# Kernel optimization log

Hardware: AMD Instinct MI355X
Metric: run time of the kernel (lower is better)

The kernel has to match this reference:

```python
import jax, jax.numpy as jnp
import numpy as np

DIM = 256
HEADS = 4
DIM_HEADS = 32
HIDDEN = HEADS * DIM_HEADS


def setup_inputs() -> dict:
    key = jax.random.key(0)
    k0, k1, k2, k3, k4, k5, k6 = jax.random.split(key, 7)
    b, c, h, w = 16, DIM, 64, 64
    s = 1.0 / np.sqrt(DIM)
    return {
        "x": jax.random.normal(k0, (b, c, h, w), dtype=jnp.float32),
        "Wq": jax.random.normal(k1, (HIDDEN, DIM), dtype=jnp.float32) * s,
        "Wk": jax.random.normal(k2, (HIDDEN, DIM), dtype=jnp.float32) * s,
        "Wv": jax.random.normal(k3, (HIDDEN, DIM), dtype=jnp.float32) * s,
        "Wo": jax.random.normal(k4, (DIM, HIDDEN), dtype=jnp.float32) / np.sqrt(HIDDEN),
        "bo": jax.random.normal(k5, (DIM,), dtype=jnp.float32) * 0.01,
        "g": jnp.ones((DIM,), dtype=jnp.float32),
    }


def reference(x, Wq, Wk, Wv, Wo, bo, g):
    b, c, h, w = x.shape
    n = h * w
    scale = DIM_HEADS ** (-0.5)
    xf = x.reshape(b, c, n)  # [b,c,n]
    # 1x1 convs == channel matmuls
    q = jnp.einsum('dc,bcn->bdn', Wq, xf).reshape(b, HEADS, DIM_HEADS, n)
    k = jnp.einsum('dc,bcn->bdn', Wk, xf).reshape(b, HEADS, DIM_HEADS, n)
    v = jnp.einsum('dc,bcn->bdn', Wv, xf).reshape(b, HEADS, DIM_HEADS, n)
    q = jax.nn.softmax(q, axis=-2) * scale  # softmax over head-dim
    k = jax.nn.softmax(k, axis=-1)          # softmax over tokens
    v = v / n
    context = jnp.einsum('bhdn,bhen->bhde', k, v)  # [b,h,dh,dh]
    out = jnp.einsum('bhde,bhdn->bhen', context, q)  # [b,h,dh,n]
    out = out.reshape(b, HIDDEN, n)
    out = jnp.einsum('cd,bdn->bcn', Wo, out) + bo[None, :, None]
    # LayerNorm over channel dim (biased var, eps=1e-5 for fp32)
    eps = 1e-5
    mean = jnp.mean(out, axis=1, keepdims=True)
    var = jnp.var(out, axis=1, keepdims=True)
    out = (out - mean) * jax.lax.rsqrt(var + eps) * g[None, :, None]
    return out.reshape(b, c, h, w)
```

## Files before the change

kernel.cpp:

```cpp
#include <hip/hip_runtime.h>
#include <hip/hip_bf16.h>

typedef float f32x4 __attribute__((ext_vector_type(4)));
typedef short bf16x8 __attribute__((ext_vector_type(8)));
typedef unsigned short us4 __attribute__((ext_vector_type(4)));

#define NB 16
#define NC 256
#define NTOK 4096
#define NHID 128

__device__ __forceinline__ unsigned pk2(float lo, float hi) {
  float2 f; f.x = lo; f.y = hi;
  __hip_bfloat162 h = __float22bfloat162_rn(f);
  unsigned u; __builtin_memcpy(&u, &h, 4); return u;
}
__device__ __forceinline__ uint2 pk4(f32x4 v) {
  uint2 r; r.x = pk2(v[0], v[1]); r.y = pk2(v[2], v[3]); return r;
}
__device__ __forceinline__ float bf2f(unsigned short h) {
  union { unsigned u; float f; } v; v.u = ((unsigned)h) << 16;
  return v.f;
}

__global__ __launch_bounds__(512) void k0_w(
    const float* __restrict__ Wq, const float* __restrict__ Wk,
    const float* __restrict__ Wv, unsigned short* __restrict__ Wswz)
{
  const int mt = blockIdx.x;
  const int t = threadIdx.x;
  const int ks = t >> 6, l = t & 63;
  const int m = mt * 16 + (l & 15);
  const int col = ks * 32 + (l >> 4) * 8;
  const float* src = (m < 128) ? (Wq + (size_t)m * NC)
                   : (m < 256) ? (Wk + (size_t)(m - 128) * NC)
                               : (Wv + (size_t)(m - 256) * NC);
  const float4 w0 = *(const float4*)(src + col);
  const float4 w1 = *(const float4*)(src + col + 4);
  uint4 p;
  p.x = pk2(w0.x, w0.y); p.y = pk2(w0.z, w0.w);
  p.z = pk2(w1.x, w1.y); p.w = pk2(w1.z, w1.w);
  *(uint4*)&Wswz[((size_t)(mt * 8 + ks)) * 512 + l * 8] = p;
}

__global__ __launch_bounds__(512, 6) void k1_qkv(
    const float* __restrict__ x, const unsigned short* __restrict__ Wswz,
    unsigned short* __restrict__ qg, unsigned short* __restrict__ Pp,
    float* __restrict__ Sp)
{
  __shared__ __align__(16) unsigned char smem[32768];

  const int tile = blockIdx.x, b = blockIdx.y;
  const int n0 = tile * 64;
  const int t = threadIdx.x;
  const int wid = t >> 6, l = t & 63;
  const int l16 = l & 15, lhi = l >> 4;
  const unsigned xr = (unsigned)((l16 & 7) << 4);

  int fr[3];
  if (wid < 4) { fr[0] = 2 * wid; fr[1] = 2 * wid + 1; fr[2] = 8 + wid; }
  else { const int w = wid - 4; fr[0] = 12 + w; fr[1] = 16 + 2 * w; fr[2] = 17 + 2 * w; }

#define WFRAG(f, kss) (*(const bf16x8*)&Wswz[((size_t)(fr[f] * 8 + (kss))) * 512 + l * 8])
#define AFRAG(tf, kss) (*(const bf16x8*)(smem + \
    (((unsigned)(((tf) * 16 + l16) * 512 + (kss) * 64 + lhi * 16)) ^ xr)))

  {
    const int cg = t >> 4;
    const int tq = t & 15;
    const float* rp = x + (size_t)b * NC * NTOK + (size_t)(cg * 8) * NTOK + n0 + tq * 4;
    float4 rv[8];
#pragma unroll
    for (int i = 0; i < 8; ++i) rv[i] = *(const float4*)(rp + (size_t)i * NTOK);
#pragma unroll
    for (int j = 0; j < 4; ++j) {
      const int tok = tq * 4 + j;
      uint4 pv;
      pv.x = pk2(rv[0][j], rv[1][j]); pv.y = pk2(rv[2][j], rv[3][j]);
      pv.z = pk2(rv[4][j], rv[5][j]); pv.w = pk2(rv[6][j], rv[7][j]);
      *(uint4*)(smem + (((unsigned)(tok * 512 + cg * 16)) ^ ((unsigned)(tok & 7) << 4))) = pv;
    }
  }
  __syncthreads();

  f32x4 acc[4][3];
#pragma unroll
  for (int i = 0; i < 4; ++i)
#pragma unroll
    for (int j = 0; j < 3; ++j) acc[i][j] = 0;

  for (int ks = 0; ks < 8; ++ks) {
    bf16x8 wf[3];
#pragma unroll
    for (int f = 0; f < 3; ++f) wf[f] = WFRAG(f, ks);
#pragma unroll
    for (int tf = 0; tf < 4; ++tf) {
      const bf16x8 a = AFRAG(tf, ks);
#pragma unroll
      for (int f = 0; f < 3; ++f)
        acc[tf][f] = __builtin_amdgcn_mfma_f32_16x16x32_bf16(a, wf[f], acc[tf][f], 0, 0, 0);
    }
  }

  const float qscale = 0.1767766952966369f;
  if (wid < 4) {
#pragma unroll
    for (int tf = 0; tf < 4; ++tf)
#pragma unroll
      for (int r = 0; r < 4; ++r) {
        const float a0 = acc[tf][0][r], a1 = acc[tf][1][r];
        float mx = fmaxf(a0, a1);
        mx = fmaxf(mx, __shfl_xor(mx, 1));
        mx = fmaxf(mx, __shfl_xor(mx, 2));
        mx = fmaxf(mx, __shfl_xor(mx, 4));
        mx = fmaxf(mx, __shfl_xor(mx, 8));
        const float e0 = __expf(a0 - mx), e1 = __expf(a1 - mx);
        float s = e0 + e1;
        s += __shfl_xor(s, 1); s += __shfl_xor(s, 2);
        s += __shfl_xor(s, 4); s += __shfl_xor(s, 8);
        const float inv = qscale / s;
        acc[tf][0][r] = e0 * inv;
        acc[tf][1][r] = e1 * inv;
      }
    float s = 0.f;
#pragma unroll
    for (int tf = 0; tf < 4; ++tf)
#pragma unroll
      for (int r = 0; r < 4; ++r) {
        const float e = __expf(acc[tf][2][r]);
        acc[tf][2][r] = e;
        s += e;
      }
    s += __shfl_xor(s, 16);
    s += __shfl_xor(s, 32);
    if (l < 16) Sp[((size_t)b * 64 + tile) * 128 + (fr[2] - 8) * 16 + l16] = s;

    unsigned short* qt = qg + ((size_t)(b * 64 + tile)) * 8192;
#pragma unroll
    for (int f = 0; f < 2; ++f) {
      const int j = fr[f] * 16 + l16;
#pragma unroll
      for (int tf = 0; tf < 4; ++tf)
        *(uint2*)&qt[tf * 2048 + j * 16 + lhi * 4] = pk4(acc[tf][f]);
    }
  } else {
    float s = 0.f;
#pragma unroll
    for (int tf = 0; tf < 4; ++tf)
#pragma unroll
      for (int r = 0; r < 4; ++r) {
        const float e = __expf(acc[tf][0][r]);
        acc[tf][0][r] = e;
        s += e;
      }
    s += __shfl_xor(s, 16);
    s += __shfl_xor(s, 32);
    if (l < 16) Sp[((size_t)b * 64 + tile) * 128 + (fr[0] - 8) * 16 + l16] = s;
  }
  __syncthreads();

  if (wid < 4) {
    const int row = (fr[2] - 8) * 16 + l16;
#pragma unroll
    for (int tf = 0; tf < 4; ++tf)
      *(uint2*)(smem + (((unsigned)(row * 128 + tf * 32 + lhi * 8)) ^ xr)) = pk4(acc[tf][2]);
  } else {
    const int rowk = (fr[0] - 8) * 16 + l16;
    const int rowv1 = 128 + (fr[1] - 16) * 16 + l16;
    const int rowv2 = 128 + (fr[2] - 16) * 16 + l16;
#pragma unroll
    for (int tf = 0; tf < 4; ++tf) {
      *(uint2*)(smem + (((unsigned)(rowk * 128 + tf * 32 + lhi * 8)) ^ xr)) = pk4(acc[tf][0]);
      *(uint2*)(smem + (((unsigned)(rowv1 * 128 + tf * 32 + lhi * 8)) ^ xr)) = pk4(acc[tf][1]);
      *(uint2*)(smem + (((unsigned)(rowv2 * 128 + tf * 32 + lhi * 8)) ^ xr)) = pk4(acc[tf][2]);
    }
  }
  __syncthreads();

  {
    const int h = wid & 3, dh = wid >> 2;
    f32x4 ca[2];
    ca[0] = 0; ca[1] = 0;
#pragma unroll
    for (int ks2 = 0; ks2 < 2; ++ks2) {
      const bf16x8 ae = *(const bf16x8*)(smem +
          (((unsigned)((h * 32 + dh * 16 + l16) * 128 + ks2 * 64 + lhi * 16)) ^ xr));
#pragma unroll
      for (int e = 0; e < 2; ++e) {
        const bf16x8 be = *(const bf16x8*)(smem +
            (((unsigned)((128 + h * 32 + e * 16 + l16) * 128 + ks2 * 64 + lhi * 16)) ^ xr));
        ca[e] = __builtin_amdgcn_mfma_f32_16x16x32_bf16(ae, be, ca[e], 0, 0, 0);
      }
    }
    unsigned short* pb = Pp + (((size_t)b * 64 + tile) * 4 + h) * 1024;
#pragma unroll
    for (int e = 0; e < 2; ++e)
      *(uint2*)&pb[(e * 16 + l16) * 32 + dh * 16 + lhi * 4] = pk4(ca[e]);
  }
}

__global__ __launch_bounds__(256) void k2a_tree(
    const unsigned short* __restrict__ Pp, const float* __restrict__ Sp,
    float* __restrict__ Pr, float* __restrict__ Sr)
{
  const int seg = blockIdx.x, b = blockIdx.y;
  const int t = threadIdx.x;
  const unsigned short* pb = Pp + ((size_t)b * 64 + seg * 8) * 4096;
  f32x4 a[4];
#pragma unroll
  for (int i = 0; i < 4; ++i) a[i] = 0;
#pragma unroll
  for (int tile = 0; tile < 8; ++tile) {
#pragma unroll
    for (int i = 0; i < 4; ++i) {
      const us4 v = *(const us4*)&pb[tile * 4096 + i * 1024 + t * 4];
      a[i][0] += bf2f(v[0]); a[i][1] += bf2f(v[1]);
      a[i][2] += bf2f(v[2]); a[i][3] += bf2f(v[3]);
    }
  }
  float* pr = Pr + ((size_t)b * 8 + seg) * 4096;
#pragma unroll
  for (int i = 0; i < 4; ++i) *(f32x4*)&pr[i * 1024 + t * 4] = a[i];

  if (t < 128) {
    float s = 0.f;
    const float* sb = Sp + ((size_t)b * 64 + seg * 8) * 128 + t;
#pragma unroll
    for (int i = 0; i < 8; ++i) s += sb[i * 128];
    Sr[((size_t)b * 8 + seg) * 128 + t] = s;
  }
}

__global__ __launch_bounds__(256) void k2bc(
    const float* __restrict__ Pr, const float* __restrict__ Sr,
    const float* __restrict__ Wo, unsigned short* __restrict__ Mswz)
{
  __shared__ float CnS[4096];
  __shared__ float Ss[128];
  const int ct = blockIdx.x, b = blockIdx.y;
  const int t = threadIdx.x;

  if (t < 128) {
    float s = 0.f;
    const float* sb = Sr + (size_t)b * 8 * 128 + t;
#pragma unroll
    for (int i = 0; i < 8; ++i) s += sb[i * 128];
    Ss[t] = 1.0f / (s * 4096.0f);
  }
  __syncthreads();

#pragma unroll
  for (int i = 0; i < 16; ++i) {
    const int idx = t + 256 * i;
    float a = 0.f;
#pragma unroll
    for (int seg = 0; seg < 8; ++seg) a += Pr[((size_t)b * 8 + seg) * 4096 + idx];
    CnS[idx] = a * Ss[((idx >> 10) << 5) | (idx & 31)];
  }
  __syncthreads();

  const int ks = t >> 6, l = t & 63;
  const int c = ct * 16 + (l & 15);
  const int d0 = (l >> 4) * 8;
  const float* wr = Wo + (size_t)c * NHID + ks * 32;
  const float* cb = &CnS[ks * 1024];
  f32x4 s0 = 0, s1 = 0;
#pragma unroll 8
  for (int e = 0; e < 32; ++e) {
    const float w = wr[e];
    const f32x4 c0 = *(const f32x4*)&cb[e * 32 + d0];
    const f32x4 c1 = *(const f32x4*)&cb[e * 32 + d0 + 4];
#pragma unroll
    for (int j = 0; j < 4; ++j) { s0[j] += w * c0[j]; s1[j] += w * c1[j]; }
  }
  uint4 p;
  p.x = pk2(s0[0], s0[1]); p.y = pk2(s0[2], s0[3]);
  p.z = pk2(s1[0], s1[1]); p.w = pk2(s1[2], s1[3]);
  *(uint4*)&Mswz[(((size_t)b * 16 + ct) * 4 + ks) * 512 + l * 8] = p;
}

__global__ __launch_bounds__(256, 3) void k3_out(
    const unsigned short* __restrict__ qg, const unsigned short* __restrict__ Mswz,
    const float* __restrict__ bo, const float* __restrict__ g, float* __restrict__ out)
{
  __shared__ __align__(16) unsigned char qs[16384];
  __shared__ float red[4 * 64 * 2];
  const int bx = blockIdx.x, b = blockIdx.y;
  const int t = threadIdx.x;
  const int wid = t >> 6, l = t & 63;
  const int l16 = l & 15, lhi = l >> 4;

  {
    const unsigned char* gq = (const unsigned char*)(qg + ((size_t)(b * 64 + bx)) * 8192);
#pragma unroll
    for (int i = 0; i < 4; ++i)
      *(uint4*)(qs + t * 16 + i * 4096) = *(const uint4*)(gq + t * 16 + i * 4096);
  }

  bf16x8 mf[4][4];
#pragma unroll
  for (int cf = 0; cf < 4; ++cf)
#pragma unroll
    for (int ks = 0; ks < 4; ++ks)
      mf[cf][ks] = *(const bf16x8*)&Mswz[(((size_t)b * 16 + wid * 4 + cf) * 4 + ks) * 512 + l * 8];

  f32x4 acc[4][4];
#pragma unroll
  for (int i = 0; i < 4; ++i)
#pragma unroll
    for (int j = 0; j < 4; ++j) acc[i][j] = 0;

  __syncthreads();

#pragma unroll
  for (int tf = 0; tf < 4; ++tf) {
    bf16x8 qf[4];
#pragma unroll
    for (int ks = 0; ks < 4; ++ks) {
      bf16x8 qv;
#pragma unroll
      for (int jj = 0; jj < 8; ++jj) {
        const unsigned short u = *(const unsigned short*)(qs +
            tf * 4096 + (ks * 32 + lhi * 8 + jj) * 32 + l16 * 2);
        qv[jj] = (short)u;
      }
      qf[ks] = qv;
    }
#pragma unroll
    for (int ks = 0; ks < 4; ++ks)
#pragma unroll
      for (int cf = 0; cf < 4; ++cf)
        acc[tf][cf] = __builtin_amdgcn_mfma_f32_16x16x32_bf16(qf[ks], mf[cf][ks], acc[tf][cf], 0, 0, 0);
  }

  float bol[4], gl[4];
#pragma unroll
  for (int cf = 0; cf < 4; ++cf) {
    const int c = wid * 64 + cf * 16 + l16;
    bol[cf] = bo[c]; gl[cf] = g[c];
  }
#pragma unroll
  for (int tf = 0; tf < 4; ++tf)
#pragma unroll
    for (int cf = 0; cf < 4; ++cf)
#pragma unroll
      for (int r = 0; r < 4; ++r) acc[tf][cf][r] += bol[cf];

  __syncthreads();

#pragma unroll
  for (int tf = 0; tf < 4; ++tf)
#pragma unroll
    for (int r = 0; r < 4; ++r) {
      float s = 0.f, q2 = 0.f;
#pragma unroll
      for (int cf = 0; cf < 4; ++cf) {
        const float v = acc[tf][cf][r];
        s += v; q2 += v * v;
      }
      s += __shfl_xor(s, 1); q2 += __shfl_xor(q2, 1);
      s += __shfl_xor(s, 2); q2 += __shfl_xor(q2, 2);
      s += __shfl_xor(s, 4); q2 += __shfl_xor(q2, 4);
      s += __shfl_xor(s, 8); q2 += __shfl_xor(q2, 8);
      if (l16 == 0) {
        const int tok = tf * 16 + lhi * 4 + r;
        red[(wid * 64 + tok) * 2] = s;
        red[(wid * 64 + tok) * 2 + 1] = q2;
      }
    }
  __syncthreads();

  float mean[4][4], rstd[4][4];
#pragma unroll
  for (int tf = 0; tf < 4; ++tf)
#pragma unroll
    for (int r = 0; r < 4; ++r) {
      const int tok = tf * 16 + lhi * 4 + r;
      float s = 0.f, q2 = 0.f;
#pragma unroll
      for (int cg = 0; cg < 4; ++cg) {
        s += red[(cg * 64 + tok) * 2];
        q2 += red[(cg * 64 + tok) * 2 + 1];
      }
      const float mu = s * (1.0f / 256.0f);
      const float var = q2 * (1.0f / 256.0f) - mu * mu;
      mean[tf][r] = mu;
      rstd[tf][r] = rsqrtf(var + 1e-5f);
    }

  float* ob = out + ((size_t)b * NC) * NTOK + bx * 64;
#pragma unroll
  for (int tf = 0; tf < 4; ++tf)
#pragma unroll
    for (int cf = 0; cf < 4; ++cf) {
      const int c = wid * 64 + cf * 16 + l16;
      f32x4 ov;
#pragma unroll
      for (int r = 0; r < 4; ++r)
        ov[r] = (acc[tf][cf][r] - mean[tf][r]) * rstd[tf][r] * gl[cf];
      *(f32x4*)&ob[(size_t)c * NTOK + tf * 16 + lhi * 4] = ov;
    }
}

extern "C" void kernel_launch(void* const* d_in, const int* in_sizes, int n_in,
                              void* d_out, int out_size, void* d_ws, size_t ws_size,
                              hipStream_t stream) {
  const float* x  = (const float*)d_in[0];
  const float* Wq = (const float*)d_in[1];
  const float* Wk = (const float*)d_in[2];
  const float* Wv = (const float*)d_in[3];
  const float* Wo = (const float*)d_in[4];
  const float* bo = (const float*)d_in[5];
  const float* g  = (const float*)d_in[6];
  float* out = (float*)d_out;

  char* ws = (char*)d_ws;
  unsigned short* Wswz = (unsigned short*)(ws);
  unsigned short* qg   = (unsigned short*)(ws + 262144);
  unsigned short* Pp   = (unsigned short*)(ws + 17039360);
  float*          Sp   = (float*)(ws + 25427968);
  float*          Pr   = (float*)(ws + 25952256);
  float*          Sr   = (float*)(ws + 28049408);
  unsigned short* Mswz = (unsigned short*)(ws + 28377088);
  (void)ws_size; (void)in_sizes; (void)n_in; (void)out_size;

  hipLaunchKernelGGL(k0_w, dim3(24), dim3(512), 0, stream, Wq, Wk, Wv, Wswz);
  hipLaunchKernelGGL(k1_qkv, dim3(64, NB), dim3(512), 0, stream, x, Wswz, qg, Pp, Sp);
  hipLaunchKernelGGL(k2a_tree, dim3(8, NB), dim3(256), 0, stream, Pp, Sp, Pr, Sr);
  hipLaunchKernelGGL(k2bc, dim3(16, NB), dim3(256), 0, stream, Pr, Sr, Wo, Mswz);
  hipLaunchKernelGGL(k3_out, dim3(64, NB), dim3(256), 0, stream, qg, Mswz, bo, g, out);
}
```

Baseline: 89.29 us.

## Split QKV tile into token halves to cut registers and raise occupancy

The QKV projection now runs in two passes over 32-token halves instead of one 64-token pass. This halves the accumulator register footprint, and the launch bound rises from 6 to 8 waves per SIMD. Each half's K/V results are written into the part of shared memory freed by the consumed x rows, using a new swizzled layout that the context MMA reads. The max subtraction in the query head-dim softmax is also dropped, which saves shuffles but could overflow exp if projections are ever large.

```diff
diff --git a/kernel.cpp b/kernel.cpp
--- a/kernel.cpp
+++ b/kernel.cpp
@@ -43,7 +43,7 @@
   *(uint4*)&Wswz[((size_t)(mt * 8 + ks)) * 512 + l * 8] = p;
 }
 
-__global__ __launch_bounds__(512, 6) void k1_qkv(
+__global__ __launch_bounds__(512, 8) void k1_qkv(
     const float* __restrict__ x, const unsigned short* __restrict__ Wswz,
     unsigned short* __restrict__ qg, unsigned short* __restrict__ Pp,
     float* __restrict__ Sp)
@@ -62,8 +62,8 @@
   else { const int w = wid - 4; fr[0] = 12 + w; fr[1] = 16 + 2 * w; fr[2] = 17 + 2 * w; }
 
 #define WFRAG(f, kss) (*(const bf16x8*)&Wswz[((size_t)(fr[f] * 8 + (kss))) * 512 + l * 8])
-#define AFRAG(tf, kss) (*(const bf16x8*)(smem + \
-    (((unsigned)(((tf) * 16 + l16) * 512 + (kss) * 64 + lhi * 16)) ^ xr)))
+#define PKV(thh, roww, offf) (smem + (unsigned)(thh) * 16384u + \
+    (((unsigned)((roww) * 64 + (offf))) ^ (((unsigned)((roww) & 7)) << 3)))
 
   {
     const int cg = t >> 4;
@@ -83,97 +83,92 @@
   }
   __syncthreads();
 
-  f32x4 acc[4][3];
-#pragma unroll
-  for (int i = 0; i < 4; ++i)
-#pragma unroll
-    for (int j = 0; j < 3; ++j) acc[i][j] = 0;
-
-  for (int ks = 0; ks < 8; ++ks) {
-    bf16x8 wf[3];
-#pragma unroll
-    for (int f = 0; f < 3; ++f) wf[f] = WFRAG(f, ks);
-#pragma unroll
-    for (int tf = 0; tf < 4; ++tf) {
-      const bf16x8 a = AFRAG(tf, ks);
-#pragma unroll
-      for (int f = 0; f < 3; ++f)
-        acc[tf][f] = __builtin_amdgcn_mfma_f32_16x16x32_bf16(a, wf[f], acc[tf][f], 0, 0, 0);
-    }
-  }
-
   const float qscale = 0.1767766952966369f;
-  if (wid < 4) {
-#pragma unroll
-    for (int tf = 0; tf < 4; ++tf)
-#pragma unroll
-      for (int r = 0; r < 4; ++r) {
-        const float a0 = acc[tf][0][r], a1 = acc[tf][1][r];
-        float mx = fmaxf(a0, a1);
-        mx = fmaxf(mx, __shfl_xor(mx, 1));
-        mx = fmaxf(mx, __shfl_xor(mx, 2));
-        mx = fmaxf(mx, __shfl_xor(mx, 4));
-        mx = fmaxf(mx, __shfl_xor(mx, 8));
-        const float e0 = __expf(a0 - mx), e1 = __expf(a1 - mx);
-        float s = e0 + e1;
-        s += __shfl_xor(s, 1); s += __shfl_xor(s, 2);
-        s += __shfl_xor(s, 4); s += __shfl_xor(s, 8);
-        const float inv = qscale / s;
-        acc[tf][0][r] = e0 * inv;
-        acc[tf][1][r] = e1 * inv;
-      }
-    float s = 0.f;
-#pragma unroll
-    for (int tf = 0; tf < 4; ++tf)
-#pragma unroll
-      for (int r = 0; r < 4; ++r) {
-        const float e = __expf(acc[tf][2][r]);
-        acc[tf][2][r] = e;
-        s += e;
-      }
-    s += __shfl_xor(s, 16);
-    s += __shfl_xor(s, 32);
-    if (l < 16) Sp[((size_t)b * 64 + tile) * 128 + (fr[2] - 8) * 16 + l16] = s;
-
-    unsigned short* qt = qg + ((size_t)(b * 64 + tile)) * 8192;
-#pragma unroll
-    for (int f = 0; f < 2; ++f) {
-      const int j = fr[f] * 16 + l16;
-#pragma unroll
-      for (int tf = 0; tf < 4; ++tf)
-        *(uint2*)&qt[tf * 2048 + j * 16 + lhi * 4] = pk4(acc[tf][f]);
-    }
-  } else {
-    float s = 0.f;
-#pragma unroll
-    for (int tf = 0; tf < 4; ++tf)
-#pragma unroll
-      for (int r = 0; r < 4; ++r) {
-        const float e = __expf(acc[tf][0][r]);
-        acc[tf][0][r] = e;
-        s += e;
-      }
-    s += __shfl_xor(s, 16);
-    s += __shfl_xor(s, 32);
-    if (l < 16) Sp[((size_t)b * 64 + tile) * 128 + (fr[0] - 8) * 16 + l16] = s;
-  }
-  __syncthreads();
-
-  if (wid < 4) {
-    const int row = (fr[2] - 8) * 16 + l16;
-#pragma unroll
-    for (int tf = 0; tf < 4; ++tf)
-      *(uint2*)(smem + (((unsigned)(row * 128 + tf * 32 + lhi * 8)) ^ xr)) = pk4(acc[tf][2]);
-  } else {
-    const int rowk = (fr[0] - 8) * 16 + l16;
-    const int rowv1 = 128 + (fr[1] - 16) * 16 + l16;
-    const int rowv2 = 128 + (fr[2] - 16) * 16 + l16;
-#pragma unroll
-    for (int tf = 0; tf < 4; ++tf) {
-      *(uint2*)(smem + (((unsigned)(rowk * 128 + tf * 32 + lhi * 8)) ^ xr)) = pk4(acc[tf][0]);
-      *(uint2*)(smem + (((unsigned)(rowv1 * 128 + tf * 32 + lhi * 8)) ^ xr)) = pk4(acc[tf][1]);
-      *(uint2*)(smem + (((unsigned)(rowv2 * 128 + tf * 32 + lhi * 8)) ^ xr)) = pk4(acc[tf][2]);
-    }
+  float ssum = 0.f;
+  unsigned short* qt = qg + ((size_t)(b * 64 + tile)) * 8192;
+
+#pragma unroll
+  for (int th = 0; th < 2; ++th) {
+    f32x4 acc[2][3];
+#pragma unroll
+    for (int i = 0; i < 2; ++i)
+#pragma unroll
+      for (int j = 0; j < 3; ++j) acc[i][j] = 0;
+
+    for (int ks = 0; ks < 8; ++ks) {
+      bf16x8 wf[3];
+#pragma unroll
+      for (int f = 0; f < 3; ++f) wf[f] = WFRAG(f, ks);
+#pragma unroll
+      for (int tf = 0; tf < 2; ++tf) {
+        const int row = th * 32 + tf * 16 + l16;
+        const bf16x8 a = *(const bf16x8*)(smem +
+            (((unsigned)(row * 512 + ks * 64 + lhi * 16)) ^ xr));
+#pragma unroll
+        for (int f = 0; f < 3; ++f)
+          acc[tf][f] = __builtin_amdgcn_mfma_f32_16x16x32_bf16(a, wf[f], acc[tf][f], 0, 0, 0);
+      }
+    }
+    __syncthreads();
+
+    if (wid < 4) {
+#pragma unroll
+      for (int tf = 0; tf < 2; ++tf)
+#pragma unroll
+        for (int r = 0; r < 4; ++r) {
+          const float e0 = __expf(acc[tf][0][r]), e1 = __expf(acc[tf][1][r]);
+          float s = e0 + e1;
+          s += __shfl_xor(s, 1); s += __shfl_xor(s, 2);
+          s += __shfl_xor(s, 4); s += __shfl_xor(s, 8);
+          const float inv = qscale / s;
+          acc[tf][0][r] = e0 * inv;
+          acc[tf][1][r] = e1 * inv;
+        }
+#pragma unroll
+      for (int tf = 0; tf < 2; ++tf)
+#pragma unroll
+        for (int r = 0; r < 4; ++r) {
+          const float e = __expf(acc[tf][2][r]);
+          acc[tf][2][r] = e;
+          ssum += e;
+        }
+#pragma unroll
+      for (int f = 0; f < 2; ++f) {
+        const int j = fr[f] * 16 + l16;
+#pragma unroll
+        for (int tf = 0; tf < 2; ++tf)
+          *(uint2*)&qt[(th * 2 + tf) * 2048 + j * 16 + lhi * 4] = pk4(acc[tf][f]);
+      }
+      const int row = (fr[2] - 8) * 16 + l16;
+#pragma unroll
+      for (int tf = 0; tf < 2; ++tf)
+        *(uint2*)PKV(th, row, tf * 32 + lhi * 8) = pk4(acc[tf][2]);
+    } else {
+#pragma unroll
+      for (int tf = 0; tf < 2; ++tf)
+#pragma unroll
+        for (int r = 0; r < 4; ++r) {
+          const float e = __expf(acc[tf][0][r]);
+          acc[tf][0][r] = e;
+          ssum += e;
+        }
+      const int rowk = (fr[0] - 8) * 16 + l16;
+      const int rowv1 = 128 + (fr[1] - 16) * 16 + l16;
+      const int rowv2 = 128 + (fr[2] - 16) * 16 + l16;
+#pragma unroll
+      for (int tf = 0; tf < 2; ++tf) {
+        *(uint2*)PKV(th, rowk, tf * 32 + lhi * 8) = pk4(acc[tf][0]);
+        *(uint2*)PKV(th, rowv1, tf * 32 + lhi * 8) = pk4(acc[tf][1]);
+        *(uint2*)PKV(th, rowv2, tf * 32 + lhi * 8) = pk4(acc[tf][2]);
+      }
+    }
+  }
+
+  ssum += __shfl_xor(ssum, 16);
+  ssum += __shfl_xor(ssum, 32);
+  {
+    const int kj = (wid < 4) ? (fr[2] - 8) : (fr[0] - 8);
+    if (l < 16) Sp[((size_t)b * 64 + tile) * 128 + kj * 16 + l16] = ssum;
   }
   __syncthreads();
 
@@ -183,12 +178,12 @@
     ca[0] = 0; ca[1] = 0;
 #pragma unroll
     for (int ks2 = 0; ks2 < 2; ++ks2) {
-      const bf16x8 ae = *(const bf16x8*)(smem +
-          (((unsigned)((h * 32 + dh * 16 + l16) * 128 + ks2 * 64 + lhi * 16)) ^ xr));
+      const int rowa = h * 32 + dh * 16 + l16;
+      const bf16x8 ae = *(const bf16x8*)PKV(ks2, rowa, lhi * 16);
 #pragma unroll
       for (int e = 0; e < 2; ++e) {
-        const bf16x8 be = *(const bf16x8*)(smem +
-            (((unsigned)((128 + h * 32 + e * 16 + l16) * 128 + ks2 * 64 + lhi * 16)) ^ xr));
+        const int rowb = 128 + h * 32 + e * 16 + l16;
+        const bf16x8 be = *(const bf16x8*)PKV(ks2, rowb, lhi * 16);
         ca[e] = __builtin_amdgcn_mfma_f32_16x16x32_bf16(ae, be, ca[e], 0, 0, 0);
       }
     }
```

Result: slower. 125.6 us (+40.6%).
